# Kernel optimization log

Measured on AMD Instinct MI355X. Metric: run time of the kernel, lower is better.

## Reference

```python
import jax, jax.numpy as jnp
import numpy as np

EPS = 1e-4  # ProtoPNet epsilon in distance-to-similarity transform


def setup_inputs() -> dict:
    key = jax.random.key(0)
    k1, k2, k3 = jax.random.split(key, 3)
    B, C, T = 128, 128, 777   # backbone feature map [B, C, T]
    P, NC = 500, 5            # prototypes, classes
    x = jax.random.normal(k1, (B, C, T), dtype=jnp.float32)
    prototypes = jax.random.uniform(k2, (P, C), dtype=jnp.float32)
    last_w = jax.random.normal(k3, (P, NC), dtype=jnp.float32)
    return {"x": x, "prototypes": prototypes, "last_w": last_w}


def reference(x, prototypes, last_w):
    # Prototype layer via the conv-trick L2 expansion:
    x2 = jnp.sum(x * x, axis=1)                      # [B, T]
    p2 = jnp.sum(prototypes * prototypes, axis=1)    # [P]
    xp = jnp.einsum('bct,pc->bpt', x, prototypes)    # [B, P, T]  (dominant GEMM)
    d = jnp.maximum(x2[:, None, :] - 2.0 * xp + p2[None, :, None], 0.0)  # [B, P, T]
    # Min-pool over all patches (global min over temporal axis)
    min_d = jnp.min(d, axis=2)                       # [B, P]
    # Distance -> similarity: log((d + 1) / (d + eps))
    sim = jnp.log((min_d + 1.0) / (min_d + EPS))     # [B, P]
    # Final evidence layer
    logits = sim @ last_w                            # [B, num_classes]
    return logits
```

## Files before the change

kernel.cpp:

```cpp
#include <hip/hip_runtime.h>
#include <hip/hip_bf16.h>

#define B_DIM 128
#define C_DIM 128
#define T_DIM 777
#define P_DIM 500
#define P_PAD 512
#define NCLS  5
#define EPSV  1e-4f
#define NTILE 13
#define SPLIT 7

typedef unsigned short u16;
typedef unsigned int   u32;
typedef __attribute__((ext_vector_type(8))) short short8;
typedef __attribute__((ext_vector_type(4))) float f32x4;
typedef float float4u __attribute__((ext_vector_type(4), aligned(4)));

__device__ __forceinline__ u32 cvt_pk_bf16(float a, float b) {
    u32 r;
    asm("v_cvt_pk_bf16_f32 %0, %1, %2" : "=v"(r) : "v"(a), "v"(b));
    return r;
}

__global__ __launch_bounds__(256, 2) void fused_gemm_min(
    const float* __restrict__ x,
    const float* __restrict__ proto,
    float* __restrict__ wsmin) {

    const int o   = blockIdx.x;
    const int xcd = o & 7, j = o >> 3;
    const int b   = xcd * 16 + (j >> 2);
    const int pt  = (j >> 1) & 1, th = j & 1;
    const int it0 = th ? SPLIT : 0;
    const int itN = th ? NTILE : SPLIT;
    const int tb0 = it0 * 64;
    const int nT  = (itN - it0) * 64;

    const int tid = threadIdx.x;
    const int w = tid >> 6, l = tid & 63;
    const int row16 = l & 15, kq = l >> 4;
    const int wp = pt * 256 + w * 64;

    const int c0  = (tid >> 3) << 2;
    const int tl0 = (tid & 7) << 2;

    __shared__ __align__(16) char  smem[64 * 256];
    __shared__ __align__(16) float x2s[448];

    const float* xb = x + (size_t)b * C_DIM * T_DIM;

    for (int i = tid; i < nT; i += 256) {
        const int t = tb0 + i;
        float a = 0.f;
        if (t < T_DIM) {
#pragma unroll 8
            for (int c = 0; c < C_DIM; ++c) {
                const float v = xb[c * T_DIM + t];
                a = fmaf(v, v, a);
            }
            x2s[i] = a;
        } else {
            x2s[i] = 1e30f;
        }
    }

    short8 afr[4][4];
#pragma unroll
    for (int ps = 0; ps < 4; ++ps) {
        const int r = wp + ps * 16 + row16;
#pragma unroll
        for (int kst = 0; kst < 4; ++kst) {
            const int k0 = kst * 32 + kq * 8;
            union { short8 s; u32 d[4]; } t;
            if (r < P_DIM) {
                float4 u0 = *(const float4*)(proto + r * C_DIM + k0);
                float4 u1 = *(const float4*)(proto + r * C_DIM + k0 + 4);
                t.d[0] = cvt_pk_bf16(u0.x, u0.y);
                t.d[1] = cvt_pk_bf16(u0.z, u0.w);
                t.d[2] = cvt_pk_bf16(u1.x, u1.y);
                t.d[3] = cvt_pk_bf16(u1.z, u1.w);
            } else {
                t.d[0] = t.d[1] = t.d[2] = t.d[3] = 0u;
            }
            afr[ps][kst] = t.s;
        }
    }

    float vb[2][4][4];
    auto loadv = [&](int it) {
#pragma unroll
        for (int h = 0; h < 2; ++h) {
            const int tb = it * 64 + h * 32 + tl0;
            if (tb + 3 < T_DIM) {
#pragma unroll
                for (int r = 0; r < 4; ++r) {
                    float4u u = *(const float4u*)(xb + (c0 + r) * T_DIM + tb);
                    vb[h][r][0]=u[0]; vb[h][r][1]=u[1]; vb[h][r][2]=u[2]; vb[h][r][3]=u[3];
                }
            } else {
#pragma unroll
                for (int r = 0; r < 4; ++r)
#pragma unroll
                    for (int jj = 0; jj < 4; ++jj) {
                        const int t = (tb + jj < T_DIM) ? (tb + jj) : (T_DIM - 1);
                        vb[h][r][jj] = xb[(c0 + r) * T_DIM + t];
                    }
            }
        }
    };

    f32x4 minv[4];
#pragma unroll
    for (int ps = 0; ps < 4; ++ps) minv[ps] = (f32x4){1e30f, 1e30f, 1e30f, 1e30f};

    __syncthreads();
    loadv(it0);

    for (int it = it0; it < itN; ++it) {
#pragma unroll
        for (int h = 0; h < 2; ++h)
#pragma unroll
            for (int jj = 0; jj < 4; ++jj) {
                const u32 lo = cvt_pk_bf16(vb[h][0][jj], vb[h][1][jj]);
                const u32 hi = cvt_pk_bf16(vb[h][2][jj], vb[h][3][jj]);
                const int tl  = h * 32 + tl0 + jj;
                const int off = tl * 256 + (((c0 >> 3) ^ (tl & 7)) << 4) + ((c0 & 4) << 1);
                *(uint2*)(smem + off) = make_uint2(lo, hi);
            }
        __syncthreads();

        if (it + 1 < itN) loadv(it + 1);

        float xv[4];
#pragma unroll
        for (int ts = 0; ts < 4; ++ts)
            xv[ts] = x2s[(it - it0) * 64 + ts * 16 + row16];

        f32x4 acc[4][4];
#pragma unroll
        for (int ps = 0; ps < 4; ++ps)
#pragma unroll
            for (int ts = 0; ts < 4; ++ts) acc[ps][ts] = (f32x4){0.f, 0.f, 0.f, 0.f};

        __builtin_amdgcn_s_setprio(1);
#pragma unroll
        for (int kst = 0; kst < 4; ++kst) {
            short8 bfr[4];
#pragma unroll
            for (int ts = 0; ts < 4; ++ts) {
                const int tl = ts * 16 + row16;
                const int gr = (kst * 4 + kq) ^ (tl & 7);
                bfr[ts] = *(const short8*)(smem + tl * 256 + (gr << 4));
            }
#pragma unroll
            for (int ps = 0; ps < 4; ++ps)
#pragma unroll
                for (int ts = 0; ts < 4; ++ts)
                    acc[ps][ts] = __builtin_amdgcn_mfma_f32_16x16x32_bf16(
                        afr[ps][kst], bfr[ts], acc[ps][ts], 0, 0, 0);
        }
        __builtin_amdgcn_s_setprio(0);

#pragma unroll
        for (int ps = 0; ps < 4; ++ps)
#pragma unroll
            for (int ts = 0; ts < 4; ++ts)
#pragma unroll
                for (int q = 0; q < 4; ++q)
                    minv[ps][q] = fminf(minv[ps][q], fmaf(-2.f, acc[ps][ts][q], xv[ts]));

        __syncthreads();
    }

#pragma unroll
    for (int m = 1; m <= 8; m <<= 1)
#pragma unroll
        for (int ps = 0; ps < 4; ++ps)
#pragma unroll
            for (int q = 0; q < 4; ++q)
                minv[ps][q] = fminf(minv[ps][q], __shfl_xor(minv[ps][q], m));

    if (row16 == 0) {
#pragma unroll
        for (int ps = 0; ps < 4; ++ps) {
            const int p = wp + ps * 16 + kq * 4;
            *(float4*)(&wsmin[((size_t)th * B_DIM + b) * P_PAD + p]) =
                make_float4(minv[ps][0], minv[ps][1], minv[ps][2], minv[ps][3]);
        }
    }
}

__global__ __launch_bounds__(256) void combine_logits(
    const float* __restrict__ proto, const float* __restrict__ lw,
    const float* __restrict__ wsmin, float* __restrict__ out) {
    const int b = blockIdx.x, tid = threadIdx.x;
    float a[NCLS] = {0.f, 0.f, 0.f, 0.f, 0.f};
    for (int p = tid; p < P_DIM; p += 256) {
        const float4* pr = (const float4*)(proto + p * C_DIM);
        float p2 = 0.f;
#pragma unroll
        for (int i = 0; i < 32; ++i) {
            float4 u = pr[i];
            p2 += u.x*u.x + u.y*u.y + u.z*u.z + u.w*u.w;
        }
        const float m0 = wsmin[(0 * B_DIM + b) * P_PAD + p];
        const float m1 = wsmin[(1 * B_DIM + b) * P_PAD + p];
        const float m  = fminf(m0, m1);
        const float md = fmaxf(m + p2, 0.f);
        const float sim = logf((md + 1.f) / (md + EPSV));
#pragma unroll
        for (int n = 0; n < NCLS; ++n) a[n] = fmaf(sim, lw[p * NCLS + n], a[n]);
    }
#pragma unroll
    for (int m = 1; m <= 32; m <<= 1)
#pragma unroll
        for (int n = 0; n < NCLS; ++n) a[n] += __shfl_xor(a[n], m);
    __shared__ float red[4][NCLS];
    const int w = tid >> 6, l = tid & 63;
    if (l == 0) {
#pragma unroll
        for (int n = 0; n < NCLS; ++n) red[w][n] = a[n];
    }
    __syncthreads();
    if (tid < NCLS)
        out[b * NCLS + tid] = red[0][tid] + red[1][tid] + red[2][tid] + red[3][tid];
}

__global__ __launch_bounds__(256) void fallback_k(const float* __restrict__ x,
                                                  const float* __restrict__ proto,
                                                  const float* __restrict__ lw,
                                                  float* __restrict__ out) {
    __shared__ float x2s[T_DIM];
    __shared__ float sims[P_DIM];
    int b = blockIdx.x, tid = threadIdx.x;
    for (int t = tid; t < T_DIM; t += 256) {
        float a = 0.f;
        for (int c = 0; c < C_DIM; ++c) { float v = x[((size_t)b * C_DIM + c) * T_DIM + t]; a = fmaf(v, v, a); }
        x2s[t] = a;
    }
    __syncthreads();
    for (int p = tid; p < P_DIM; p += 256) {
        float p2 = 0.f;
        for (int c = 0; c < C_DIM; ++c) { float v = proto[p * C_DIM + c]; p2 = fmaf(v, v, p2); }
        float mind = 1e30f;
        for (int t = 0; t < T_DIM; ++t) {
            float xp = 0.f;
            for (int c = 0; c < C_DIM; ++c)
                xp = fmaf(x[((size_t)b * C_DIM + c) * T_DIM + t], proto[p * C_DIM + c], xp);
            float d = fmaxf(x2s[t] - 2.f * xp + p2, 0.f);
            mind = fminf(mind, d);
        }
        sims[p] = logf((mind + 1.f) / (mind + EPSV));
    }
    __syncthreads();
    if (tid < NCLS) {
        float a = 0.f;
        for (int p = 0; p < P_DIM; ++p) a = fmaf(sims[p], lw[p * NCLS + tid], a);
        out[b * NCLS + tid] = a;
    }
}

extern "C" void kernel_launch(void* const* d_in, const int* in_sizes, int n_in,
                              void* d_out, int out_size, void* d_ws, size_t ws_size,
                              hipStream_t stream) {
    const float* x     = (const float*)d_in[0];
    const float* proto = (const float*)d_in[1];
    const float* lw    = (const float*)d_in[2];
    float* out = (float*)d_out;

    const size_t need = (size_t)2 * B_DIM * P_PAD * sizeof(float);

    if (ws_size >= need) {
        float* wsmin = (float*)d_ws;
        fused_gemm_min<<<dim3(512), 256, 0, stream>>>(x, proto, wsmin);
        combine_logits<<<dim3(B_DIM), 256, 0, stream>>>(proto, lw, wsmin, out);
    } else {
        fallback_k<<<dim3(B_DIM), 256, 0, stream>>>(x, proto, lw, out);
    }
}
```

Measured before the change: 48.76 us.

## Merge prototype halves into 512-thread blocks and fuse x-norm into tile staging

Each block now covers all 512 prototypes with 8 waves, so each x tile is loaded and converted once per block instead of twice. The grid halves to 256 blocks. The separate strided pass that computed ||x||^2 per timestep is replaced by partial sums taken from the staged registers, reduced with shuffles and a small shared buffer. The loop is reordered so the next tile is written after the min-update, with one extra barrier per iteration. This removes a redundant read of x and the serial column-norm loop, but fewer blocks may reduce occupancy or latency hiding.

```diff
diff --git a/kernel.cpp b/kernel.cpp
--- a/kernel.cpp
+++ b/kernel.cpp
@@ -9,7 +9,7 @@
 #define NCLS  5
 #define EPSV  1e-4f
 #define NTILE 13
-#define SPLIT 7
+#define SPL   7
 
 typedef unsigned short u16;
 typedef unsigned int   u32;
@@ -23,59 +23,87 @@
     return r;
 }
 
-__global__ __launch_bounds__(256, 2) void fused_gemm_min(
+__global__ __launch_bounds__(512, 2) void fused_gemm_min(
     const float* __restrict__ x,
     const float* __restrict__ proto,
     float* __restrict__ wsmin) {
 
     const int o   = blockIdx.x;
     const int xcd = o & 7, j = o >> 3;
-    const int b   = xcd * 16 + (j >> 2);
-    const int pt  = (j >> 1) & 1, th = j & 1;
-    const int it0 = th ? SPLIT : 0;
-    const int itN = th ? NTILE : SPLIT;
-    const int tb0 = it0 * 64;
-    const int nT  = (itN - it0) * 64;
+    const int b   = xcd * 16 + (j >> 1);
+    const int th  = j & 1;
+    const int it0 = th ? SPL : 0;
+    const int itN = th ? NTILE : SPL;
 
     const int tid = threadIdx.x;
     const int w = tid >> 6, l = tid & 63;
     const int row16 = l & 15, kq = l >> 4;
-    const int wp = pt * 256 + w * 64;
-
-    const int c0  = (tid >> 3) << 2;
-    const int tl0 = (tid & 7) << 2;
+    const int wp = w * 64;
+
+    const int c0  = (tid >> 4) << 2;
+    const int tl0 = (tid & 15) << 2;
 
     __shared__ __align__(16) char  smem[64 * 256];
-    __shared__ __align__(16) float x2s[448];
+    __shared__ __align__(16) float x2p[8][64];
+    __shared__ __align__(16) float x2f[64];
 
     const float* xb = x + (size_t)b * C_DIM * T_DIM;
 
-    for (int i = tid; i < nT; i += 256) {
-        const int t = tb0 + i;
-        float a = 0.f;
-        if (t < T_DIM) {
-#pragma unroll 8
-            for (int c = 0; c < C_DIM; ++c) {
-                const float v = xb[c * T_DIM + t];
-                a = fmaf(v, v, a);
+    float vb[4][4];
+    auto loadv = [&](int it) {
+        const int tb = it * 64 + tl0;
+        if (tb + 3 < T_DIM) {
+#pragma unroll
+            for (int r = 0; r < 4; ++r) {
+                float4u u = *(const float4u*)(xb + (c0 + r) * T_DIM + tb);
+                vb[r][0]=u[0]; vb[r][1]=u[1]; vb[r][2]=u[2]; vb[r][3]=u[3];
             }
-            x2s[i] = a;
         } else {
-            x2s[i] = 1e30f;
-        }
-    }
+#pragma unroll
+            for (int r = 0; r < 4; ++r)
+#pragma unroll
+                for (int jj = 0; jj < 4; ++jj) {
+                    const int t = (tb + jj < T_DIM) ? (tb + jj) : (T_DIM - 1);
+                    vb[r][jj] = xb[(c0 + r) * T_DIM + t];
+                }
+        }
+    };
+
+    auto write_tile = [&]() {
+        float s[4];
+#pragma unroll
+        for (int jj = 0; jj < 4; ++jj)
+            s[jj] = vb[0][jj]*vb[0][jj] + vb[1][jj]*vb[1][jj]
+                  + vb[2][jj]*vb[2][jj] + vb[3][jj]*vb[3][jj];
+#pragma unroll
+        for (int jj = 0; jj < 4; ++jj) {
+            const u32 lo = cvt_pk_bf16(vb[0][jj], vb[1][jj]);
+            const u32 hi = cvt_pk_bf16(vb[2][jj], vb[3][jj]);
+            const int tl  = tl0 + jj;
+            const int off = tl * 256 + (((c0 >> 3) ^ (tl & 7)) << 4) + ((c0 & 4) << 1);
+            *(uint2*)(smem + off) = make_uint2(lo, hi);
+        }
+#pragma unroll
+        for (int m = 16; m <= 32; m <<= 1)
+#pragma unroll
+            for (int jj = 0; jj < 4; ++jj) s[jj] += __shfl_xor(s[jj], m);
+        if (l < 16)
+            *(float4*)(&x2p[w][tl0]) = make_float4(s[0], s[1], s[2], s[3]);
+    };
+
+    loadv(it0);
 
     short8 afr[4][4];
 #pragma unroll
     for (int ps = 0; ps < 4; ++ps) {
-        const int r = wp + ps * 16 + row16;
-#pragma unroll
-        for (int kst = 0; kst < 4; ++kst) {
-            const int k0 = kst * 32 + kq * 8;
+        const int rr = wp + ps * 16 + row16;
+#pragma unroll
+        for (int k = 0; k < 4; ++k) {
+            const int k0 = k * 32 + kq * 8;
             union { short8 s; u32 d[4]; } t;
-            if (r < P_DIM) {
-                float4 u0 = *(const float4*)(proto + r * C_DIM + k0);
-                float4 u1 = *(const float4*)(proto + r * C_DIM + k0 + 4);
+            if (rr < P_DIM) {
+                float4 u0 = *(const float4*)(proto + rr * C_DIM + k0);
+                float4 u1 = *(const float4*)(proto + rr * C_DIM + k0 + 4);
                 t.d[0] = cvt_pk_bf16(u0.x, u0.y);
                 t.d[1] = cvt_pk_bf16(u0.z, u0.w);
                 t.d[2] = cvt_pk_bf16(u1.x, u1.y);
@@ -83,59 +111,27 @@
             } else {
                 t.d[0] = t.d[1] = t.d[2] = t.d[3] = 0u;
             }
-            afr[ps][kst] = t.s;
-        }
-    }
-
-    float vb[2][4][4];
-    auto loadv = [&](int it) {
-#pragma unroll
-        for (int h = 0; h < 2; ++h) {
-            const int tb = it * 64 + h * 32 + tl0;
-            if (tb + 3 < T_DIM) {
-#pragma unroll
-                for (int r = 0; r < 4; ++r) {
-                    float4u u = *(const float4u*)(xb + (c0 + r) * T_DIM + tb);
-                    vb[h][r][0]=u[0]; vb[h][r][1]=u[1]; vb[h][r][2]=u[2]; vb[h][r][3]=u[3];
-                }
-            } else {
-#pragma unroll
-                for (int r = 0; r < 4; ++r)
-#pragma unroll
-                    for (int jj = 0; jj < 4; ++jj) {
-                        const int t = (tb + jj < T_DIM) ? (tb + jj) : (T_DIM - 1);
-                        vb[h][r][jj] = xb[(c0 + r) * T_DIM + t];
-                    }
-            }
-        }
-    };
+            afr[ps][k] = t.s;
+        }
+    }
 
     f32x4 minv[4];
 #pragma unroll
     for (int ps = 0; ps < 4; ++ps) minv[ps] = (f32x4){1e30f, 1e30f, 1e30f, 1e30f};
 
-    __syncthreads();
-    loadv(it0);
+    write_tile();
+    __syncthreads();
 
     for (int it = it0; it < itN; ++it) {
-#pragma unroll
-        for (int h = 0; h < 2; ++h)
-#pragma unroll
-            for (int jj = 0; jj < 4; ++jj) {
-                const u32 lo = cvt_pk_bf16(vb[h][0][jj], vb[h][1][jj]);
-                const u32 hi = cvt_pk_bf16(vb[h][2][jj], vb[h][3][jj]);
-                const int tl  = h * 32 + tl0 + jj;
-                const int off = tl * 256 + (((c0 >> 3) ^ (tl & 7)) << 4) + ((c0 & 4) << 1);
-                *(uint2*)(smem + off) = make_uint2(lo, hi);
-            }
-        __syncthreads();
-
-        if (it + 1 < itN) loadv(it + 1);
-
-        float xv[4];
-#pragma unroll
-        for (int ts = 0; ts < 4; ++ts)
-            xv[ts] = x2s[(it - it0) * 64 + ts * 16 + row16];
+        const bool more = (it + 1 < itN);
+        if (more) loadv(it + 1);
+
+        if (w == 0) {
+            const int t = it * 64 + l;
+            float sum = x2p[0][l] + x2p[1][l] + x2p[2][l] + x2p[3][l]
+                      + x2p[4][l] + x2p[5][l] + x2p[6][l] + x2p[7][l];
+            x2f[l] = (t < T_DIM) ? sum : 1e30f;
+        }
 
         f32x4 acc[4][4];
 #pragma unroll
@@ -162,6 +158,11 @@
         }
         __builtin_amdgcn_s_setprio(0);
 
+        __syncthreads();
+
+        float xv[4];
+#pragma unroll
+        for (int ts = 0; ts < 4; ++ts) xv[ts] = x2f[ts * 16 + row16];
 #pragma unroll
         for (int ps = 0; ps < 4; ++ps)
 #pragma unroll
@@ -170,7 +171,10 @@
                 for (int q = 0; q < 4; ++q)
                     minv[ps][q] = fminf(minv[ps][q], fmaf(-2.f, acc[ps][ts][q], xv[ts]));
 
-        __syncthreads();
+        if (more) {
+            write_tile();
+            __syncthreads();
+        }
     }
 
 #pragma unroll
@@ -204,8 +208,8 @@
             float4 u = pr[i];
             p2 += u.x*u.x + u.y*u.y + u.z*u.z + u.w*u.w;
         }
-        const float m0 = wsmin[(0 * B_DIM + b) * P_PAD + p];
-        const float m1 = wsmin[(1 * B_DIM + b) * P_PAD + p];
+        const float m0 = wsmin[((size_t)0 * B_DIM + b) * P_PAD + p];
+        const float m1 = wsmin[((size_t)1 * B_DIM + b) * P_PAD + p];
         const float m  = fminf(m0, m1);
         const float md = fmaxf(m + p2, 0.f);
         const float sim = logf((md + 1.f) / (md + EPSV));
@@ -273,7 +277,7 @@
 
     if (ws_size >= need) {
         float* wsmin = (float*)d_ws;
-        fused_gemm_min<<<dim3(512), 256, 0, stream>>>(x, proto, wsmin);
+        fused_gemm_min<<<dim3(256), 512, 0, stream>>>(x, proto, wsmin);
         combine_logits<<<dim3(B_DIM), 256, 0, stream>>>(proto, lw, wsmin, out);
     } else {
         fallback_k<<<dim3(B_DIM), 256, 0, stream>>>(x, proto, lw, out);
```

Result: faster. 43.63 us (-10.5%).
